# Optimization experiments

Hardware: AMD Instinct MI355X
Metric: run time of the kernel (lower is better)

The kernel has to match this reference:

```python
import jax, jax.numpy as jnp
import numpy as np

B, H, W, C = 2, 384, 384, 32
KH = KW = 3
K = KH * KW
F = 32


def setup_inputs() -> dict:
    key = jax.random.key(0)
    k1, k2, k3 = jax.random.split(key, 3)
    x = jax.random.normal(k1, (B, H, W, C), dtype=jnp.float32)
    # distortion offsets (x_off, y_off) per output pixel per kernel tap, shared over batch
    offset = jax.random.normal(k2, (1, H, W, K, 2), dtype=jnp.float32)
    kernel = jax.random.normal(k3, (K, C, F), dtype=jnp.float32) * (1.0 / np.sqrt(K * C))
    bias = jnp.zeros((F,), dtype=jnp.float32)
    return {"x": x, "offset": offset, "kernel": kernel, "bias": bias}


def _deform_bilinear_sample(x, offset):
    # x: [B,H,W,C] NHWC; offset: [1,H,W,K,2] with channel 0 = x_off, 1 = y_off
    b, h_in, w_in, c = x.shape
    pad = (KH - 1) // 2  # SAME padding for 3x3 stride 1
    xp = jnp.pad(x, ((0, 0), (pad, pad), (pad, pad), (0, 0)))
    hp, wp = h_in + 2 * pad, w_in + 2 * pad

    # base sampling grid in padded coordinates: output (i,j), tap (di,dj) -> (i+di, j+dj)
    yb = (jnp.arange(h_in)[:, None, None, None] + jnp.arange(KH)[None, None, :, None])  # [H,1,KH,1]
    xb = (jnp.arange(w_in)[None, :, None, None] + jnp.arange(KW)[None, None, None, :])  # [1,W,1,KW]
    yb = jnp.broadcast_to(yb, (h_in, w_in, KH, KW)).reshape(h_in, w_in, K)
    xb = jnp.broadcast_to(xb, (h_in, w_in, KH, KW)).reshape(h_in, w_in, K)

    x_off = offset[0, ..., 0]  # [H,W,K]
    y_off = offset[0, ..., 1]
    yf = jnp.clip(yb.astype(jnp.float32) + y_off, 0.0, hp - 1)
    xf = jnp.clip(xb.astype(jnp.float32) + x_off, 0.0, wp - 1)

    y0 = jnp.floor(yf).astype(jnp.int32)
    x0 = jnp.floor(xf).astype(jnp.int32)
    y1 = jnp.clip(y0 + 1, 0, hp - 1)
    x1 = jnp.clip(x0 + 1, 0, wp - 1)
    y0 = jnp.clip(y0, 0, hp - 1)
    x0 = jnp.clip(x0, 0, wp - 1)

    def gather(yi, xi):
        # indices shared across batch -> [B,H,W,K,C]
        return xp[:, yi, xi, :]

    p0 = gather(y0, x0)
    p1 = gather(y0, x1)
    p2 = gather(y1, x0)
    p3 = gather(y1, x1)

    y0f, x0f, y1f, x1f = (y0.astype(jnp.float32), x0.astype(jnp.float32),
                          y1.astype(jnp.float32), x1.astype(jnp.float32))
    w0 = ((y1f - yf) * (x1f - xf))[..., None]
    w1 = ((y1f - yf) * (xf - x0f))[..., None]
    w2 = ((yf - y0f) * (x1f - xf))[..., None]
    w3 = ((yf - y0f) * (xf - x0f))[..., None]
    # [B,H,W,K,C]
    return w0 * p0 + w1 * p1 + w2 * p2 + w3 * p3


def reference(x, offset, kernel, bias):
    pixels = _deform_bilinear_sample(x, offset)  # [B,H,W,K,C]
    # depthwise-conv trick + sum over input channels == dense contraction over (K, C)
    out = jnp.einsum('bhwkc,kcf->bhwf', pixels, kernel) + bias
    return out
```

## Files before the change

### kernel.cpp

```cpp
#include <hip/hip_runtime.h>

typedef short short8 __attribute__((ext_vector_type(8)));
typedef float f32x4 __attribute__((ext_vector_type(4)));
typedef unsigned int uint4v __attribute__((ext_vector_type(4)));

#define H_ 384
#define W_ 384
#define C_ 32
#define HW_ 147456
#define HP1F 385.0f
#define NB 2

__device__ __forceinline__ unsigned short f2bf(float f) {
  unsigned int u = __float_as_uint(f);
  u += 0x7fffu + ((u >> 16) & 1u);
  return (unsigned short)(u >> 16);
}

__device__ __forceinline__ unsigned pack2(float a, float b) {
  return (unsigned)f2bf(a) | ((unsigned)f2bf(b) << 16);
}

__device__ __forceinline__ void issue_tap(
    const float* __restrict__ x, float2 oA, float2 oB,
    int i, int di, int jA, int jB, int dj, int b, int c0,
    float& wA00, float& wA01, float& wA10, float& wA11,
    float& wB00, float& wB01, float& wB10, float& wB11,
    f32x4& cA00, f32x4& cA01, f32x4& cA10, f32x4& cA11,
    f32x4& cB00, f32x4& cB01, f32x4& cB10, f32x4& cB11) {
  float yfA = (float)(i + di) + oA.y;
  float xfA = (float)(jA + dj) + oA.x;
  yfA = fminf(fmaxf(yfA, 0.f), HP1F);
  xfA = fminf(fmaxf(xfA, 0.f), HP1F);
  const float y0fA = floorf(yfA), x0fA = floorf(xfA);
  const int y0A = (int)y0fA, x0A = (int)x0fA;

  float yfB = (float)(i + di) + oB.y;
  float xfB = (float)(jB + dj) + oB.x;
  yfB = fminf(fmaxf(yfB, 0.f), HP1F);
  xfB = fminf(fmaxf(xfB, 0.f), HP1F);
  const float y0fB = floorf(yfB), x0fB = floorf(xfB);
  const int y0B = (int)y0fB, x0B = (int)x0fB;

  const int fastA = ((unsigned)(y0A - 1) < 383u) & ((unsigned)(x0A - 1) < 383u);
  const int fastB = ((unsigned)(y0B - 1) < 383u) & ((unsigned)(x0B - 1) < 383u);

  if (__all(fastA & fastB)) {
    const float wy1A = yfA - y0fA, wy0A = (y0fA + 1.0f) - yfA;
    const float wx1A = xfA - x0fA, wx0A = (x0fA + 1.0f) - xfA;
    wA00 = wy0A * wx0A; wA01 = wy0A * wx1A;
    wA10 = wy1A * wx0A; wA11 = wy1A * wx1A;
    const float wy1B = yfB - y0fB, wy0B = (y0fB + 1.0f) - yfB;
    const float wx1B = xfB - x0fB, wx0B = (x0fB + 1.0f) - xfB;
    wB00 = wy0B * wx0B; wB01 = wy0B * wx1B;
    wB10 = wy1B * wx0B; wB11 = wy1B * wx1B;

    const int baseA = ((b * H_ + (y0A - 1)) * W_ + (x0A - 1)) * C_ + c0;
    const int baseB = ((b * H_ + (y0B - 1)) * W_ + (x0B - 1)) * C_ + c0;
    cA00 = *(const f32x4*)(x + baseA);
    cA01 = *(const f32x4*)(x + baseA + C_);
    cA10 = *(const f32x4*)(x + baseA + W_ * C_);
    cA11 = *(const f32x4*)(x + baseA + W_ * C_ + C_);
    cB00 = *(const f32x4*)(x + baseB);
    cB01 = *(const f32x4*)(x + baseB + C_);
    cB10 = *(const f32x4*)(x + baseB + W_ * C_);
    cB11 = *(const f32x4*)(x + baseB + W_ * C_ + C_);
  } else {
    const f32x4 z = {0.f, 0.f, 0.f, 0.f};
    {
      const int y1 = min(y0A + 1, 385);
      const int x1 = min(x0A + 1, 385);
      const float wy1 = yfA - y0fA, wy0 = (float)y1 - yfA;
      const float wx1 = xfA - x0fA, wx0 = (float)x1 - xfA;
      wA00 = wy0 * wx0; wA01 = wy0 * wx1;
      wA10 = wy1 * wx0; wA11 = wy1 * wx1;
      const int yu0 = y0A - 1, xu0 = x0A - 1;
      const bool vy0 = (unsigned)yu0 < 384u, vy1 = (unsigned)(y1 - 1) < 384u;
      const bool vx0 = (unsigned)xu0 < 384u, vx1 = (unsigned)(x1 - 1) < 384u;
      const int base00 = ((b * H_ + yu0) * W_ + xu0) * C_ + c0;
      const int ddx = (x1 - x0A) * C_;
      const int ddy = (y1 - y0A) * (W_ * C_);
      cA00 = z; cA01 = z; cA10 = z; cA11 = z;
      if (vy0 && vx0) cA00 = *(const f32x4*)(x + base00);
      if (vy0 && vx1) cA01 = *(const f32x4*)(x + base00 + ddx);
      if (vy1 && vx0) cA10 = *(const f32x4*)(x + base00 + ddy);
      if (vy1 && vx1) cA11 = *(const f32x4*)(x + base00 + ddy + ddx);
    }
    {
      const int y1 = min(y0B + 1, 385);
      const int x1 = min(x0B + 1, 385);
      const float wy1 = yfB - y0fB, wy0 = (float)y1 - yfB;
      const float wx1 = xfB - x0fB, wx0 = (float)x1 - xfB;
      wB00 = wy0 * wx0; wB01 = wy0 * wx1;
      wB10 = wy1 * wx0; wB11 = wy1 * wx1;
      const int yu0 = y0B - 1, xu0 = x0B - 1;
      const bool vy0 = (unsigned)yu0 < 384u, vy1 = (unsigned)(y1 - 1) < 384u;
      const bool vx0 = (unsigned)xu0 < 384u, vx1 = (unsigned)(x1 - 1) < 384u;
      const int base00 = ((b * H_ + yu0) * W_ + xu0) * C_ + c0;
      const int ddx = (x1 - x0B) * C_;
      const int ddy = (y1 - y0B) * (W_ * C_);
      cB00 = z; cB01 = z; cB10 = z; cB11 = z;
      if (vy0 && vx0) cB00 = *(const f32x4*)(x + base00);
      if (vy0 && vx1) cB01 = *(const f32x4*)(x + base00 + ddx);
      if (vy1 && vx0) cB10 = *(const f32x4*)(x + base00 + ddy);
      if (vy1 && vx1) cB11 = *(const f32x4*)(x + base00 + ddy + ddx);
    }
  }
}

__global__ __launch_bounds__(256) void deform_conv_kernel(
    const float* __restrict__ x, const float* __restrict__ off,
    const float* __restrict__ kern, const float* __restrict__ bias,
    float* __restrict__ out) {
  __shared__ short ldsB[9216];

  const int tid = threadIdx.x;
  const int lane = tid & 63;

  {
    unsigned short* pk = (unsigned short*)ldsB;
    for (int e = tid; e < 1152; e += 256) {
      const int ln = e & 63;
      const int kk = (e >> 6) % 9;
      const int nt = e / 576;
      const int f = nt * 16 + (ln & 15);
      const int q2 = ln >> 4;
      unsigned short rr[8];
#pragma unroll
      for (int i2 = 0; i2 < 8; ++i2) {
        const int c = q2 * 8 + i2;
        rr[i2] = f2bf(kern[(kk * 32 + c) * 32 + f]);
      }
      uint4 w;
      w.x = rr[0] | ((unsigned)rr[1] << 16);
      w.y = rr[2] | ((unsigned)rr[3] << 16);
      w.z = rr[4] | ((unsigned)rr[5] << 16);
      w.w = rr[6] | ((unsigned)rr[7] << 16);
      *(uint4*)&pk[e * 8] = w;
    }
    __syncthreads();
  }
  const short8* bp = (const short8*)ldsB;

  const float bias0 = bias[lane & 15];
  const float bias1 = bias[16 + (lane & 15)];

  const int q  = lane >> 3;
  const int cq = lane & 7;
  const int c0 = cq * 4;

  const int mrow = lane & 15;
  const int qq = lane >> 4;
  const int sl0 = (((mrow & 7) << 3) + (qq << 1)) << 2;
  const int sl1 = sl0 + 4;
  const bool hi = (mrow & 8) != 0;

  const int lb = (blockIdx.x & 7) * 288 + (blockIdx.x >> 3);

  for (int nb = 0; nb < NB; ++nb) {
    const int g = lb * (4 * NB) + nb * 4 + (tid >> 6);
    const int P0 = g << 4;
    const int b = (P0 >= HW_) ? 1 : 0;
    const int rem = P0 - b * HW_;
    const int i = rem / W_;
    const int j0 = rem - i * W_;
    const int jA = j0 + q;
    const int jB = j0 + 8 + q;

    const float* opixA = off + (size_t)(i * W_ + jA) * 18;
    const float* opixB = off + (size_t)(i * W_ + jB) * 18;

    f32x4 acc0 = {bias0, bias0, bias0, bias0};
    f32x4 acc1 = {bias1, bias1, bias1, bias1};

    float wA00, wA01, wA10, wA11, wB00, wB01, wB10, wB11;
    f32x4 cA00, cA01, cA10, cA11, cB00, cB01, cB10, cB11;
    float nA00, nA01, nA10, nA11, nB00, nB01, nB10, nB11;
    f32x4 dA00, dA01, dA10, dA11, dB00, dB01, dB10, dB11;

    float2 oA = *(const float2*)(opixA);
    float2 oB = *(const float2*)(opixB);
    issue_tap(x, oA, oB, i, 0, jA, jB, 0, b, c0,
              wA00, wA01, wA10, wA11, wB00, wB01, wB10, wB11,
              cA00, cA01, cA10, cA11, cB00, cB01, cB10, cB11);
    float2 oA1 = *(const float2*)(opixA + 2);
    float2 oB1 = *(const float2*)(opixB + 2);

#pragma unroll
    for (int kk = 0; kk < 9; ++kk) {
      const f32x4 vA = wA00 * cA00 + wA01 * cA01 + wA10 * cA10 + wA11 * cA11;
      const f32x4 vB = wB00 * cB00 + wB01 * cB01 + wB10 * cB10 + wB11 * cB11;

      if (kk < 8) {
        const int di1 = (kk + 1) / 3;
        const int dj1 = (kk + 1) - di1 * 3;
        issue_tap(x, oA1, oB1, i, di1, jA, jB, dj1, b, c0,
                  nA00, nA01, nA10, nA11, nB00, nB01, nB10, nB11,
                  dA00, dA01, dA10, dA11, dB00, dB01, dB10, dB11);
      }
      if (kk < 7) {
        oA1 = *(const float2*)(opixA + (kk + 2) * 2);
        oB1 = *(const float2*)(opixB + (kk + 2) * 2);
      }

      const int a0 = (int)pack2(vA[0], vA[1]);
      const int a1 = (int)pack2(vA[2], vA[3]);
      const int b0 = (int)pack2(vB[0], vB[1]);
      const int b1 = (int)pack2(vB[2], vB[3]);

      const int pa0 = __builtin_amdgcn_ds_bpermute(sl0, a0);
      const int pb0 = __builtin_amdgcn_ds_bpermute(sl0, b0);
      const int pa1 = __builtin_amdgcn_ds_bpermute(sl0, a1);
      const int pb1 = __builtin_amdgcn_ds_bpermute(sl0, b1);
      const int pa2 = __builtin_amdgcn_ds_bpermute(sl1, a0);
      const int pb2 = __builtin_amdgcn_ds_bpermute(sl1, b0);
      const int pa3 = __builtin_amdgcn_ds_bpermute(sl1, a1);
      const int pb3 = __builtin_amdgcn_ds_bpermute(sl1, b1);
      const uint4v uu = {(unsigned)(hi ? pb0 : pa0), (unsigned)(hi ? pb1 : pa1),
                         (unsigned)(hi ? pb2 : pa2), (unsigned)(hi ? pb3 : pa3)};
      const short8 af = __builtin_bit_cast(short8, uu);

      acc0 = __builtin_amdgcn_mfma_f32_16x16x32_bf16(af, bp[kk * 64 + lane], acc0, 0, 0, 0);
      acc1 = __builtin_amdgcn_mfma_f32_16x16x32_bf16(af, bp[(9 + kk) * 64 + lane], acc1, 0, 0, 0);

      if (kk < 8) {
        wA00 = nA00; wA01 = nA01; wA10 = nA10; wA11 = nA11;
        wB00 = nB00; wB01 = nB01; wB10 = nB10; wB11 = nB11;
        cA00 = dA00; cA01 = dA01; cA10 = dA10; cA11 = dA11;
        cB00 = dB00; cB01 = dB01; cB10 = dB10; cB11 = dB11;
      }
    }

    float* op = out + (size_t)(P0 + qq * 4) * 32 + (lane & 15);
#pragma unroll
    for (int r = 0; r < 4; ++r) {
      op[r * 32] = acc0[r];
      op[r * 32 + 16] = acc1[r];
    }
  }
}

extern "C" void kernel_launch(void* const* d_in, const int* in_sizes, int n_in,
                              void* d_out, int out_size, void* d_ws, size_t ws_size,
                              hipStream_t stream) {
  const float* x    = (const float*)d_in[0];
  const float* off  = (const float*)d_in[1];
  const float* kern = (const float*)d_in[2];
  const float* bias = (const float*)d_in[3];
  float* out = (float*)d_out;
  deform_conv_kernel<<<dim3(2304), dim3(256), 0, stream>>>(x, off, kern, bias, out);
}
```

Measured before the change: 168.1 us.

## Pre-convert input to bf16 in workspace and gather bf16 corners

Adds a pre-pass kernel that converts x to bf16 in the workspace, plus a new deform-conv kernel that gathers the four bilinear corners as 8-byte bf16 loads instead of fp32. This halves the gather bytes and cache footprint of the random-access corner reads, at the cost of an extra launch and a full read and write of x. Corner values now lose precision before interpolation rather than only after. It falls back to the old kernel if the workspace is too small.

```diff
diff --git a/kernel.cpp b/kernel.cpp
--- a/kernel.cpp
+++ b/kernel.cpp
@@ -10,6 +10,7 @@
 #define HW_ 147456
 #define HP1F 385.0f
 #define NB 2
+#define XB_ELEMS 9437184
 
 __device__ __forceinline__ unsigned short f2bf(float f) {
   unsigned int u = __float_as_uint(f);
@@ -20,6 +21,250 @@
 __device__ __forceinline__ unsigned pack2(float a, float b) {
   return (unsigned)f2bf(a) | ((unsigned)f2bf(b) << 16);
 }
+
+__device__ __forceinline__ f32x4 b4_to_f(uint2 r) {
+  f32x4 v;
+  v[0] = __uint_as_float(r.x << 16);
+  v[1] = __uint_as_float(r.x & 0xffff0000u);
+  v[2] = __uint_as_float(r.y << 16);
+  v[3] = __uint_as_float(r.y & 0xffff0000u);
+  return v;
+}
+
+
+__device__ __forceinline__ void issue_tap_b(
+    const unsigned short* __restrict__ xb, float2 oA, float2 oB,
+    int i, int di, int jA, int jB, int dj, int b, int c0,
+    float& wA00, float& wA01, float& wA10, float& wA11,
+    float& wB00, float& wB01, float& wB10, float& wB11,
+    uint2& rA00, uint2& rA01, uint2& rA10, uint2& rA11,
+    uint2& rB00, uint2& rB01, uint2& rB10, uint2& rB11) {
+  float yfA = (float)(i + di) + oA.y;
+  float xfA = (float)(jA + dj) + oA.x;
+  yfA = fminf(fmaxf(yfA, 0.f), HP1F);
+  xfA = fminf(fmaxf(xfA, 0.f), HP1F);
+  const float y0fA = floorf(yfA), x0fA = floorf(xfA);
+  const int y0A = (int)y0fA, x0A = (int)x0fA;
+
+  float yfB = (float)(i + di) + oB.y;
+  float xfB = (float)(jB + dj) + oB.x;
+  yfB = fminf(fmaxf(yfB, 0.f), HP1F);
+  xfB = fminf(fmaxf(xfB, 0.f), HP1F);
+  const float y0fB = floorf(yfB), x0fB = floorf(xfB);
+  const int y0B = (int)y0fB, x0B = (int)x0fB;
+
+  const int fastA = ((unsigned)(y0A - 1) < 383u) & ((unsigned)(x0A - 1) < 383u);
+  const int fastB = ((unsigned)(y0B - 1) < 383u) & ((unsigned)(x0B - 1) < 383u);
+
+  if (__all(fastA & fastB)) {
+    const float wy1A = yfA - y0fA, wy0A = (y0fA + 1.0f) - yfA;
+    const float wx1A = xfA - x0fA, wx0A = (x0fA + 1.0f) - xfA;
+    wA00 = wy0A * wx0A; wA01 = wy0A * wx1A;
+    wA10 = wy1A * wx0A; wA11 = wy1A * wx1A;
+    const float wy1B = yfB - y0fB, wy0B = (y0fB + 1.0f) - yfB;
+    const float wx1B = xfB - x0fB, wx0B = (x0fB + 1.0f) - xfB;
+    wB00 = wy0B * wx0B; wB01 = wy0B * wx1B;
+    wB10 = wy1B * wx0B; wB11 = wy1B * wx1B;
+
+    const int baseA = ((b * H_ + (y0A - 1)) * W_ + (x0A - 1)) * C_ + c0;
+    const int baseB = ((b * H_ + (y0B - 1)) * W_ + (x0B - 1)) * C_ + c0;
+    rA00 = *(const uint2*)(xb + baseA);
+    rA01 = *(const uint2*)(xb + baseA + C_);
+    rA10 = *(const uint2*)(xb + baseA + W_ * C_);
+    rA11 = *(const uint2*)(xb + baseA + W_ * C_ + C_);
+    rB00 = *(const uint2*)(xb + baseB);
+    rB01 = *(const uint2*)(xb + baseB + C_);
+    rB10 = *(const uint2*)(xb + baseB + W_ * C_);
+    rB11 = *(const uint2*)(xb + baseB + W_ * C_ + C_);
+  } else {
+    const uint2 z = {0u, 0u};
+    {
+      const int y1 = min(y0A + 1, 385);
+      const int x1 = min(x0A + 1, 385);
+      const float wy1 = yfA - y0fA, wy0 = (float)y1 - yfA;
+      const float wx1 = xfA - x0fA, wx0 = (float)x1 - xfA;
+      wA00 = wy0 * wx0; wA01 = wy0 * wx1;
+      wA10 = wy1 * wx0; wA11 = wy1 * wx1;
+      const int yu0 = y0A - 1, xu0 = x0A - 1;
+      const bool vy0 = (unsigned)yu0 < 384u, vy1 = (unsigned)(y1 - 1) < 384u;
+      const bool vx0 = (unsigned)xu0 < 384u, vx1 = (unsigned)(x1 - 1) < 384u;
+      const int base00 = ((b * H_ + yu0) * W_ + xu0) * C_ + c0;
+      const int ddx = (x1 - x0A) * C_;
+      const int ddy = (y1 - y0A) * (W_ * C_);
+      rA00 = z; rA01 = z; rA10 = z; rA11 = z;
+      if (vy0 && vx0) rA00 = *(const uint2*)(xb + base00);
+      if (vy0 && vx1) rA01 = *(const uint2*)(xb + base00 + ddx);
+      if (vy1 && vx0) rA10 = *(const uint2*)(xb + base00 + ddy);
+      if (vy1 && vx1) rA11 = *(const uint2*)(xb + base00 + ddy + ddx);
+    }
+    {
+      const int y1 = min(y0B + 1, 385);
+      const int x1 = min(x0B + 1, 385);
+      const float wy1 = yfB - y0fB, wy0 = (float)y1 - yfB;
+      const float wx1 = xfB - x0fB, wx0 = (float)x1 - xfB;
+      wB00 = wy0 * wx0; wB01 = wy0 * wx1;
+      wB10 = wy1 * wx0; wB11 = wy1 * wx1;
+      const int yu0 = y0B - 1, xu0 = x0B - 1;
+      const bool vy0 = (unsigned)yu0 < 384u, vy1 = (unsigned)(y1 - 1) < 384u;
+      const bool vx0 = (unsigned)xu0 < 384u, vx1 = (unsigned)(x1 - 1) < 384u;
+      const int base00 = ((b * H_ + yu0) * W_ + xu0) * C_ + c0;
+      const int ddx = (x1 - x0B) * C_;
+      const int ddy = (y1 - y0B) * (W_ * C_);
+      rB00 = z; rB01 = z; rB10 = z; rB11 = z;
+      if (vy0 && vx0) rB00 = *(const uint2*)(xb + base00);
+      if (vy0 && vx1) rB01 = *(const uint2*)(xb + base00 + ddx);
+      if (vy1 && vx0) rB10 = *(const uint2*)(xb + base00 + ddy);
+      if (vy1 && vx1) rB11 = *(const uint2*)(xb + base00 + ddy + ddx);
+    }
+  }
+}
+
+__global__ __launch_bounds__(256) void deform_conv_b16(
+    const unsigned short* __restrict__ xb, const float* __restrict__ off,
+    const float* __restrict__ kern, const float* __restrict__ bias,
+    float* __restrict__ out) {
+  __shared__ short ldsB[9216];
+
+  const int tid = threadIdx.x;
+  const int lane = tid & 63;
+
+  {
+    unsigned short* pk = (unsigned short*)ldsB;
+    for (int e = tid; e < 1152; e += 256) {
+      const int ln = e & 63;
+      const int kk = (e >> 6) % 9;
+      const int nt = e / 576;
+      const int f = nt * 16 + (ln & 15);
+      const int q2 = ln >> 4;
+      unsigned short rr[8];
+#pragma unroll
+      for (int i2 = 0; i2 < 8; ++i2) {
+        const int c = q2 * 8 + i2;
+        rr[i2] = f2bf(kern[(kk * 32 + c) * 32 + f]);
+      }
+      uint4 w;
+      w.x = rr[0] | ((unsigned)rr[1] << 16);
+      w.y = rr[2] | ((unsigned)rr[3] << 16);
+      w.z = rr[4] | ((unsigned)rr[5] << 16);
+      w.w = rr[6] | ((unsigned)rr[7] << 16);
+      *(uint4*)&pk[e * 8] = w;
+    }
+    __syncthreads();
+  }
+  const short8* bp = (const short8*)ldsB;
+
+  const float bias0 = bias[lane & 15];
+  const float bias1 = bias[16 + (lane & 15)];
+
+  const int q  = lane >> 3;
+  const int cq = lane & 7;
+  const int c0 = cq * 4;
+
+  const int mrow = lane & 15;
+  const int qq = lane >> 4;
+  const int sl0 = (((mrow & 7) << 3) + (qq << 1)) << 2;
+  const int sl1 = sl0 + 4;
+  const bool hi = (mrow & 8) != 0;
+
+  const int lb = (blockIdx.x & 7) * 288 + (blockIdx.x >> 3);
+
+  for (int nb = 0; nb < NB; ++nb) {
+    const int g = lb * (4 * NB) + nb * 4 + (tid >> 6);
+    const int P0 = g << 4;
+    const int b = (P0 >= HW_) ? 1 : 0;
+    const int rem = P0 - b * HW_;
+    const int i = rem / W_;
+    const int j0 = rem - i * W_;
+    const int jA = j0 + q;
+    const int jB = j0 + 8 + q;
+
+    const float* opixA = off + (size_t)(i * W_ + jA) * 18;
+    const float* opixB = off + (size_t)(i * W_ + jB) * 18;
+
+    f32x4 acc0 = {bias0, bias0, bias0, bias0};
+    f32x4 acc1 = {bias1, bias1, bias1, bias1};
+
+    float wA00, wA01, wA10, wA11, wB00, wB01, wB10, wB11;
+    uint2 rA00, rA01, rA10, rA11, rB00, rB01, rB10, rB11;
+    float nA00, nA01, nA10, nA11, nB00, nB01, nB10, nB11;
+    uint2 sA00, sA01, sA10, sA11, sB00, sB01, sB10, sB11;
+
+    float2 oA = *(const float2*)(opixA);
+    float2 oB = *(const float2*)(opixB);
+    issue_tap_b(xb, oA, oB, i, 0, jA, jB, 0, b, c0,
+                wA00, wA01, wA10, wA11, wB00, wB01, wB10, wB11,
+                rA00, rA01, rA10, rA11, rB00, rB01, rB10, rB11);
+    float2 oA1 = *(const float2*)(opixA + 2);
+    float2 oB1 = *(const float2*)(opixB + 2);
+
+#pragma unroll
+    for (int kk = 0; kk < 9; ++kk) {
+      const f32x4 vA = wA00 * b4_to_f(rA00) + wA01 * b4_to_f(rA01)
+                     + wA10 * b4_to_f(rA10) + wA11 * b4_to_f(rA11);
+      const f32x4 vB = wB00 * b4_to_f(rB00) + wB01 * b4_to_f(rB01)
+                     + wB10 * b4_to_f(rB10) + wB11 * b4_to_f(rB11);
+
+      if (kk < 8) {
+        const int di1 = (kk + 1) / 3;
+        const int dj1 = (kk + 1) - di1 * 3;
+        issue_tap_b(xb, oA1, oB1, i, di1, jA, jB, dj1, b, c0,
+                    nA00, nA01, nA10, nA11, nB00, nB01, nB10, nB11,
+                    sA00, sA01, sA10, sA11, sB00, sB01, sB10, sB11);
+      }
+      if (kk < 7) {
+        oA1 = *(const float2*)(opixA + (kk + 2) * 2);
+        oB1 = *(const float2*)(opixB + (kk + 2) * 2);
+      }
+
+      const int a0 = (int)pack2(vA[0], vA[1]);
+      const int a1 = (int)pack2(vA[2], vA[3]);
+      const int b0 = (int)pack2(vB[0], vB[1]);
+      const int b1 = (int)pack2(vB[2], vB[3]);
+
+      const int pa0 = __builtin_amdgcn_ds_bpermute(sl0, a0);
+      const int pb0 = __builtin_amdgcn_ds_bpermute(sl0, b0);
+      const int pa1 = __builtin_amdgcn_ds_bpermute(sl0, a1);
+      const int pb1 = __builtin_amdgcn_ds_bpermute(sl0, b1);
+      const int pa2 = __builtin_amdgcn_ds_bpermute(sl1, a0);
+      const int pb2 = __builtin_amdgcn_ds_bpermute(sl1, b0);
+      const int pa3 = __builtin_amdgcn_ds_bpermute(sl1, a1);
+      const int pb3 = __builtin_amdgcn_ds_bpermute(sl1, b1);
+      const uint4v uu = {(unsigned)(hi ? pb0 : pa0), (unsigned)(hi ? pb1 : pa1),
+                         (unsigned)(hi ? pb2 : pa2), (unsigned)(hi ? pb3 : pa3)};
+      const short8 af = __builtin_bit_cast(short8, uu);
+
+      acc0 = __builtin_amdgcn_mfma_f32_16x16x32_bf16(af, bp[kk * 64 + lane], acc0, 0, 0, 0);
+      acc1 = __builtin_amdgcn_mfma_f32_16x16x32_bf16(af, bp[(9 + kk) * 64 + lane], acc1, 0, 0, 0);
+
+      if (kk < 8) {
+        wA00 = nA00; wA01 = nA01; wA10 = nA10; wA11 = nA11;
+        wB00 = nB00; wB01 = nB01; wB10 = nB10; wB11 = nB11;
+        rA00 = sA00; rA01 = sA01; rA10 = sA10; rA11 = sA11;
+        rB00 = sB00; rB01 = sB01; rB10 = sB10; rB11 = sB11;
+      }
+    }
+
+    float* op = out + (size_t)(P0 + qq * 4) * 32 + (lane & 15);
+#pragma unroll
+    for (int r = 0; r < 4; ++r) {
+      op[r * 32] = acc0[r];
+      op[r * 32 + 16] = acc1[r];
+    }
+  }
+}
+
+__global__ __launch_bounds__(256) void cvt_bf16_kernel(
+    const float* __restrict__ x, unsigned short* __restrict__ xb) {
+  const int n4 = XB_ELEMS / 4;
+  for (int t = blockIdx.x * 256 + threadIdx.x; t < n4; t += gridDim.x * 256) {
+    const float4 v = ((const float4*)x)[t];
+    uint2 w;
+    w.x = pack2(v.x, v.y);
+    w.y = pack2(v.z, v.w);
+    ((uint2*)xb)[t] = w;
+  }
+}
+
 
 __device__ __forceinline__ void issue_tap(
     const float* __restrict__ x, float2 oA, float2 oB,
@@ -248,5 +493,13 @@
   const float* kern = (const float*)d_in[2];
   const float* bias = (const float*)d_in[3];
   float* out = (float*)d_out;
-  deform_conv_kernel<<<dim3(2304), dim3(256), 0, stream>>>(x, off, kern, bias, out);
-}
+
+  const size_t xb_bytes = (size_t)XB_ELEMS * 2;
+  if (d_ws != nullptr && ws_size >= xb_bytes) {
+    unsigned short* xb = (unsigned short*)d_ws;
+    cvt_bf16_kernel<<<dim3(2048), dim3(256), 0, stream>>>(x, xb);
+    deform_conv_b16<<<dim3(2304), dim3(256), 0, stream>>>(xb, off, kern, bias, out);
+  } else {
+    deform_conv_kernel<<<dim3(2304), dim3(256), 0, stream>>>(x, off, kern, bias, out);
+  }
+}
```

Measured after the change: 170.5 us. No clear change (+1.4%).

## Pre-convert input to padded bf16 buffer and gather from it

Applied to the files above, without the earlier changes.

Adds a pre-pass kernel that converts the fp32 NHWC input into a zero-padded bf16 copy in workspace. The main kernel then gathers bilinear corners as 16-byte bf16 vectors with no bounds checks, which halves gather bytes and removes the per-sample conversion. The cost is an extra launch plus a full read and write of the input every call. Corner values are now rounded to bf16 before interpolation, so the error differs from before, and the new path runs only when the workspace is large enough.

```diff
diff --git a/kernel.cpp b/kernel.cpp
--- a/kernel.cpp
+++ b/kernel.cpp
@@ -10,6 +10,10 @@
 #define HW_ 147456
 #define HP1F 385.0f
 #define NB 2
+#define PW 386
+#define PROW (PW * C_)
+#define XPAD_ELEMS (2 * PW * PW * C_)
+#define XPAD_BYTES ((size_t)XPAD_ELEMS * 2)
 
 __device__ __forceinline__ unsigned short f2bf(float f) {
   unsigned int u = __float_as_uint(f);
@@ -20,6 +24,175 @@
 __device__ __forceinline__ unsigned pack2(float a, float b) {
   return (unsigned)f2bf(a) | ((unsigned)f2bf(b) << 16);
 }
+
+__device__ __forceinline__ void b8_to_f(uint4 r, f32x4& lo, f32x4& hi) {
+  lo[0] = __uint_as_float(r.x << 16);
+  lo[1] = __uint_as_float(r.x & 0xffff0000u);
+  lo[2] = __uint_as_float(r.y << 16);
+  lo[3] = __uint_as_float(r.y & 0xffff0000u);
+  hi[0] = __uint_as_float(r.z << 16);
+  hi[1] = __uint_as_float(r.z & 0xffff0000u);
+  hi[2] = __uint_as_float(r.w << 16);
+  hi[3] = __uint_as_float(r.w & 0xffff0000u);
+}
+
+
+__device__ __forceinline__ void issue_tap_d(
+    const unsigned short* __restrict__ xb, float2 o,
+    int i, int di, int j, int dj, int b, int c0,
+    float& w00, float& w01, float& w10, float& w11,
+    uint4& r00, uint4& r01, uint4& r10, uint4& r11) {
+  float yf = (float)(i + di) + o.y;
+  float xf = (float)(j + dj) + o.x;
+  yf = fminf(fmaxf(yf, 0.f), HP1F);
+  xf = fminf(fmaxf(xf, 0.f), HP1F);
+  const float y0f = floorf(yf), x0f = floorf(xf);
+  const int y0 = (int)y0f, x0 = (int)x0f;
+  const int y1 = min(y0 + 1, 385), x1 = min(x0 + 1, 385);
+  const float wy1 = yf - y0f, wy0 = (float)y1 - yf;
+  const float wx1 = xf - x0f, wx0 = (float)x1 - xf;
+  w00 = wy0 * wx0; w01 = wy0 * wx1;
+  w10 = wy1 * wx0; w11 = wy1 * wx1;
+  const int base = ((b * PW + y0) * PW + x0) * C_ + c0;
+  const int dx = (x1 - x0) * C_;
+  const int dy = (y1 - y0) * PROW;
+  r00 = *(const uint4*)(xb + base);
+  r01 = *(const uint4*)(xb + base + dx);
+  r10 = *(const uint4*)(xb + base + dy);
+  r11 = *(const uint4*)(xb + base + dy + dx);
+}
+
+__global__ __launch_bounds__(256) void deform_conv_d(
+    const unsigned short* __restrict__ xb, const float* __restrict__ off,
+    const float* __restrict__ kern, const float* __restrict__ bias,
+    float* __restrict__ out) {
+  __shared__ short ldsB[9216];
+
+  const int tid = threadIdx.x;
+  const int lane = tid & 63;
+
+  {
+    unsigned short* pk = (unsigned short*)ldsB;
+    for (int e = tid; e < 1152; e += 256) {
+      const int ln = e & 63;
+      const int kk = (e >> 6) % 9;
+      const int nt = e / 576;
+      const int f = nt * 16 + (ln & 15);
+      const int q2 = ln >> 4;
+      unsigned short rr[8];
+#pragma unroll
+      for (int i2 = 0; i2 < 8; ++i2) {
+        const int c = q2 * 8 + i2;
+        rr[i2] = f2bf(kern[(kk * 32 + c) * 32 + f]);
+      }
+      uint4 w;
+      w.x = rr[0] | ((unsigned)rr[1] << 16);
+      w.y = rr[2] | ((unsigned)rr[3] << 16);
+      w.z = rr[4] | ((unsigned)rr[5] << 16);
+      w.w = rr[6] | ((unsigned)rr[7] << 16);
+      *(uint4*)&pk[e * 8] = w;
+    }
+    __syncthreads();
+  }
+  const short8* bp = (const short8*)ldsB;
+
+  const float bias0 = bias[lane & 15];
+  const float bias1 = bias[16 + (lane & 15)];
+
+  const int mrow = lane & 15;
+  const int qq = lane >> 4;
+  const int c0 = qq * 8;
+
+  const int lb = (blockIdx.x & 7) * 288 + (blockIdx.x >> 3);
+
+  for (int nb = 0; nb < NB; ++nb) {
+    const int g = lb * (4 * NB) + nb * 4 + (tid >> 6);
+    const int P0 = g << 4;
+    const int b = (P0 >= HW_) ? 1 : 0;
+    const int rem = P0 - b * HW_;
+    const int i = rem / W_;
+    const int j0 = rem - i * W_;
+    const int j = j0 + mrow;
+
+    const float* opix = off + (size_t)(i * W_ + j) * 18;
+
+    f32x4 acc0 = {bias0, bias0, bias0, bias0};
+    f32x4 acc1 = {bias1, bias1, bias1, bias1};
+
+    float wc00, wc01, wc10, wc11;
+    uint4 rc00, rc01, rc10, rc11;
+    float wn00, wn01, wn10, wn11;
+    uint4 rn00, rn01, rn10, rn11;
+
+    float2 oc = *(const float2*)(opix);
+    issue_tap_d(xb, oc, i, 0, j, 0, b, c0,
+                wc00, wc01, wc10, wc11, rc00, rc01, rc10, rc11);
+    float2 o1 = *(const float2*)(opix + 2);
+
+#pragma unroll
+    for (int kk = 0; kk < 9; ++kk) {
+      f32x4 l00, h00, l01, h01, l10, h10, l11, h11;
+      b8_to_f(rc00, l00, h00);
+      b8_to_f(rc01, l01, h01);
+      b8_to_f(rc10, l10, h10);
+      b8_to_f(rc11, l11, h11);
+      const f32x4 vlo = wc00 * l00 + wc01 * l01 + wc10 * l10 + wc11 * l11;
+      const f32x4 vhi = wc00 * h00 + wc01 * h01 + wc10 * h10 + wc11 * h11;
+
+      if (kk < 8) {
+        const int di1 = (kk + 1) / 3;
+        const int dj1 = (kk + 1) - di1 * 3;
+        issue_tap_d(xb, o1, i, di1, j, dj1, b, c0,
+                    wn00, wn01, wn10, wn11, rn00, rn01, rn10, rn11);
+      }
+      if (kk < 7) o1 = *(const float2*)(opix + (kk + 2) * 2);
+
+      const uint4v uu = {pack2(vlo[0], vlo[1]), pack2(vlo[2], vlo[3]),
+                         pack2(vhi[0], vhi[1]), pack2(vhi[2], vhi[3])};
+      const short8 af = __builtin_bit_cast(short8, uu);
+
+      acc0 = __builtin_amdgcn_mfma_f32_16x16x32_bf16(af, bp[kk * 64 + lane], acc0, 0, 0, 0);
+      acc1 = __builtin_amdgcn_mfma_f32_16x16x32_bf16(af, bp[(9 + kk) * 64 + lane], acc1, 0, 0, 0);
+
+      if (kk < 8) {
+        wc00 = wn00; wc01 = wn01; wc10 = wn10; wc11 = wn11;
+        rc00 = rn00; rc01 = rn01; rc10 = rn10; rc11 = rn11;
+      }
+    }
+
+    float* op = out + (size_t)(P0 + qq * 4) * 32 + (lane & 15);
+#pragma unroll
+    for (int r = 0; r < 4; ++r) {
+      op[r * 32] = acc0[r];
+      op[r * 32 + 16] = acc1[r];
+    }
+  }
+}
+
+__global__ __launch_bounds__(256) void cvt_pad_kernel(
+    const float* __restrict__ x, unsigned short* __restrict__ xb) {
+  const int total = 2 * PW * PW * 4;
+  for (int t = blockIdx.x * 256 + threadIdx.x; t < total; t += gridDim.x * 256) {
+    const int c8 = t & 3;
+    const int p  = t >> 2;
+    const int xp = p % PW;
+    const int yp = (p / PW) % PW;
+    const int b  = p / (PW * PW);
+    uint4 w = {0u, 0u, 0u, 0u};
+    const unsigned py = (unsigned)(yp - 1), px = (unsigned)(xp - 1);
+    if (py < 384u && px < 384u) {
+      const float* src = x + (((size_t)(b * H_ + (int)py) * W_ + (int)px) * C_ + c8 * 8);
+      const float4 v0 = *(const float4*)(src);
+      const float4 v1 = *(const float4*)(src + 4);
+      w.x = pack2(v0.x, v0.y);
+      w.y = pack2(v0.z, v0.w);
+      w.z = pack2(v1.x, v1.y);
+      w.w = pack2(v1.z, v1.w);
+    }
+    *(uint4*)(xb + ((size_t)p * C_ + c8 * 8)) = w;
+  }
+}
+
 
 __device__ __forceinline__ void issue_tap(
     const float* __restrict__ x, float2 oA, float2 oB,
@@ -248,5 +421,12 @@
   const float* kern = (const float*)d_in[2];
   const float* bias = (const float*)d_in[3];
   float* out = (float*)d_out;
-  deform_conv_kernel<<<dim3(2304), dim3(256), 0, stream>>>(x, off, kern, bias, out);
-}
+
+  if (d_ws != nullptr && ws_size >= XPAD_BYTES) {
+    unsigned short* xb = (unsigned short*)d_ws;
+    cvt_pad_kernel<<<dim3(2048), dim3(256), 0, stream>>>(x, xb);
+    deform_conv_d<<<dim3(2304), dim3(256), 0, stream>>>(xb, off, kern, bias, out);
+  } else {
+    deform_conv_kernel<<<dim3(2304), dim3(256), 0, stream>>>(x, off, kern, bias, out);
+  }
+}
```

New measurement: 153.9 us, median of 3. 8.5% less time.
